# Kernel optimization log

Hardware: AMD Instinct MI355X
Metric: run time of the kernel (lower is better)

Reference implementation:

```python
import jax, jax.numpy as jnp
import numpy as np

N_NODES = 10000
N_EDGES = 320000
MUL = 32            # multiplicity of each input/output irrep
RADIAL = 8          # edge scalar (radial basis) dim
HID = 64            # fc_neurons widths
NUM_NEIGHBORS = 32.0
MIX = np.pi / 8.0
INV_SQRT2 = 1.0 / np.sqrt(2.0)   # per-path alpha: 2 paths feed each mid irrep
INV_SQRT3 = 1.0 / np.sqrt(3.0)   # w3j(1,1,0) normalization


def setup_inputs() -> dict:
    key = jax.random.key(0)
    ks = jax.random.split(key, 16)
    inp = {
        "node_input": jax.random.normal(ks[0], (N_NODES, 4 * MUL), jnp.float32),  # 32x0e+32x1o flat
        "edge_attr": jax.random.normal(ks[1], (N_EDGES, 4), jnp.float32),          # 1x0e+1x1o (sh l=0,1)
        "edge_scalar_attr": jax.random.uniform(ks[2], (N_EDGES, RADIAL), jnp.float32),
        # first linear: 32x0e+32x1o -> (32x0e+32x1o) + (32x0e+32x1o); columns [:MUL]=conv path, [MUL:]=self path
        "W1_0e": jax.random.normal(ks[3], (MUL, 2 * MUL), jnp.float32),
        "W1_1o": jax.random.normal(ks[4], (MUL, 2 * MUL), jnp.float32),
        # radial MLP
        "W_mlp1": jax.random.normal(ks[5], (RADIAL, HID), jnp.float32),
        "W_mlp2": jax.random.normal(ks[6], (HID, HID), jnp.float32),
        # per-instruction 'uvu' path weights (mul_v = 1 squeezed): shape (HID, MUL)
        "Wp_00": jax.random.normal(ks[7], (HID, MUL), jnp.float32),  # 0e x 0e -> 0e
        "Wp_01": jax.random.normal(ks[8], (HID, MUL), jnp.float32),  # 0e x 1o -> 1o
        "Wp_10": jax.random.normal(ks[9], (HID, MUL), jnp.float32),  # 1o x 0e -> 1o
        "Wp_11": jax.random.normal(ks[10], (HID, MUL), jnp.float32), # 1o x 1o -> 0e
        # final linear: 64x0e+64x1o -> 32x0e+32x1o
        "W2_0e": jax.random.normal(ks[11], (2 * MUL, MUL), jnp.float32),
        "W2_1o": jax.random.normal(ks[12], (2 * MUL, MUL), jnp.float32),
        "edge_src": jax.random.randint(ks[13], (N_EDGES,), 0, N_NODES, jnp.int32),
        "edge_dst": jax.random.randint(ks[14], (N_EDGES,), 0, N_NODES, jnp.int32),
    }
    return inp


def _forward(node_input, edge_attr, edge_scalar_attr,
             W1_0e, W1_1o, W_mlp1, W_mlp2,
             Wp_00, Wp_01, Wp_10, Wp_11, W2_0e, W2_1o,
             edge_src, edge_dst):
    N = node_input.shape[0]
    # split flat node features into irrep blocks: 32x0e (N,32), 32x1o (N,32,3)
    x0 = node_input[:, :MUL]
    x1 = node_input[:, MUL:].reshape(N, MUL, 3)

    # ---- equivariant Linear: input -> input + output (fan-in normalized) ----
    f0 = (x0 @ W1_0e) / np.sqrt(MUL)                           # (N, 2*MUL)
    f1 = jnp.einsum('nui,uw->nwi', x1, W1_1o) / np.sqrt(MUL)   # (N, 2*MUL, 3)
    feat0, self0 = f0[:, :MUL], f0[:, MUL:]
    feat1, self1 = f1[:, :MUL], f1[:, MUL:]

    # ---- gather to edges ----
    e0 = feat0[edge_src]        # (E, MUL)
    e1 = feat1[edge_src]        # (E, MUL, 3)
    ea0 = edge_attr[:, :1]      # (E, 1) 0e
    ea1 = edge_attr[:, 1:4]     # (E, 3) 1o

    # ---- radial MLP -> per-edge per-path weights ----
    h = jax.nn.gelu((edge_scalar_attr @ W_mlp1) / np.sqrt(RADIAL))
    h = jax.nn.gelu((h @ W_mlp2) / np.sqrt(HID))               # (E, HID)
    w00 = h @ Wp_00   # (E, MUL)
    w01 = h @ Wp_01
    w10 = h @ Wp_10
    w11 = h @ Wp_11

    # ---- CG tensor product, 'uvu' mode (mul_v = 1) ----
    out0_a = w00 * e0 * ea0                                   # 0e x 0e -> 0e   (E, MUL)
    out0_b = w11 * jnp.sum(e1 * ea1[:, None, :], -1) * INV_SQRT3  # 1o.1o -> 0e
    out1_a = (w01 * e0)[:, :, None] * ea1[:, None, :]         # 0e x 1o -> 1o   (E, MUL, 3)
    out1_b = (w10[:, :, None] * e1) * ea0[:, :, None]         # 1o x 0e -> 1o
    mid0 = jnp.concatenate([out0_a, out0_b], axis=1) * INV_SQRT2  # (E, 2*MUL)   64x0e
    mid1 = jnp.concatenate([out1_a, out1_b], axis=1) * INV_SQRT2  # (E, 2*MUL, 3) 64x1o

    # ---- scatter-add to destination nodes ----
    n0 = jax.ops.segment_sum(mid0, edge_dst, num_segments=N) / np.sqrt(NUM_NEIGHBORS)
    n1 = jax.ops.segment_sum(mid1, edge_dst, num_segments=N) / np.sqrt(NUM_NEIGHBORS)

    # ---- final equivariant Linear: 64x0e+64x1o -> 32x0e+32x1o ----
    conv0 = (n0 @ W2_0e) / np.sqrt(2 * MUL)                    # (N, MUL)
    conv1 = jnp.einsum('nui,uw->nwi', n1, W2_1o) / np.sqrt(2 * MUL)  # (N, MUL, 3)

    c, s = np.cos(MIX), np.sin(MIX)
    y0 = c * self0 + s * conv0
    y1 = c * self1 + s * conv1
    return jnp.concatenate([y0, y1.reshape(N, MUL * 3)], axis=1)  # (N, 128)


def reference(node_input, edge_attr, edge_scalar_attr,
              W1_0e, W1_1o, W_mlp1, W_mlp2,
              Wp_00, Wp_01, Wp_10, Wp_11, W2_0e, W2_1o,
              edge_src, edge_dst):
    return _forward(node_input, edge_attr, edge_scalar_attr,
                    W1_0e, W1_1o, W_mlp1, W_mlp2,
                    Wp_00, Wp_01, Wp_10, Wp_11, W2_0e, W2_1o,
                    edge_src, edge_dst)
```

## Files before the change

### kernel.cpp

```cpp
#include <hip/hip_runtime.h>

typedef unsigned int uint32;
typedef __attribute__((ext_vector_type(4))) float f32x4;
typedef __attribute__((ext_vector_type(8))) _Float16 halfx8;
typedef __attribute__((ext_vector_type(4))) uint32 uint32x4;

#define N_NODES 10000
#define N_EDGES 320000

#define SC_W1      0.17677669529663687f
#define SC_MLP1    0.35355339059327373f
#define SC_MLP2    0.125f
#define INV_SQRT3  0.5773502691896258f
#define COS_MIX    0.9238795325112867f
#define SIN_CONV   0.04783542904563623f

#define WS_FEATP 0
#define I_CNT    1280000
#define I_OFF    1290016
#define U_REC    1300032
#define U_WF     2580032
#define U_WBUF   2587200

__device__ __forceinline__ uint32 f2bf(float x) {
    uint32 u = __float_as_uint(x);
    return (u + 0x7fffu + ((u >> 16) & 1u)) >> 16;
}
__device__ __forceinline__ uint32 pack_bf2(float a, float b) {
    return f2bf(a) | (f2bf(b) << 16);
}
__device__ __forceinline__ uint32 packh2(float a, float b) {
    _Float16 ha = (_Float16)a, hb = (_Float16)b;
    return (uint32)__builtin_bit_cast(unsigned short, ha) |
           ((uint32)__builtin_bit_cast(unsigned short, hb) << 16);
}
__device__ __forceinline__ unsigned short h16(float x) {
    _Float16 h = (_Float16)x;
    return __builtin_bit_cast(unsigned short, h);
}
__device__ __forceinline__ float gelu_fast(float x) {
    float x2 = x * x;
    float z = x * __builtin_fmaf(0.03567740814f, x2, 0.7978845608f);
    float E = __builtin_amdgcn_exp2f(z * -2.885390082f);
    return x * __builtin_amdgcn_rcpf(1.0f + E);
}

#define K1_NODE_BLOCKS 2500
#define K1_CNT_BLOCKS  1250
#define K1_PREP_BLOCKS 7
__global__ __launch_bounds__(256) void k1_fused(
        const float* __restrict__ x,
        const float* __restrict__ W1_0e, const float* __restrict__ W1_1o,
        const int* __restrict__ edge_dst, int* __restrict__ cnt,
        const float* __restrict__ Wm1, const float* __restrict__ Wm2,
        const float* __restrict__ Wp00, const float* __restrict__ Wp01,
        const float* __restrict__ Wp10, const float* __restrict__ Wp11,
        uint32* __restrict__ wf,
        float* __restrict__ featp, float* __restrict__ out) {
    int b = blockIdx.x;
    if (b < K1_NODE_BLOCKS) {
        __shared__ float xrow[4][128];
        int wv = threadIdx.x >> 6, lane = threadIdx.x & 63;
        int node = b * 4 + wv;
        float2 v = *(const float2*)(x + (size_t)node * 128 + lane * 2);
        xrow[wv][lane * 2]     = v.x;
        xrow[wv][lane * 2 + 1] = v.y;
        __syncthreads();
        const float* sx = xrow[wv];
        int w = lane;
        float f0 = 0.f, f1x = 0.f, f1y = 0.f, f1z = 0.f;
#pragma unroll
        for (int u = 0; u < 32; ++u) {
            float w0 = W1_0e[u * 64 + w];
            float w1 = W1_1o[u * 64 + w];
            f0  += sx[u] * w0;
            f1x += sx[32 + u * 3 + 0] * w1;
            f1y += sx[32 + u * 3 + 1] * w1;
            f1z += sx[32 + u * 3 + 2] * w1;
        }
        f0 *= SC_W1; f1x *= SC_W1; f1y *= SC_W1; f1z *= SC_W1;
        if (w < 32) {
            featp[node * 128 + w]      = f0;
            featp[node * 128 + 32 + w] = f1x;
            featp[node * 128 + 64 + w] = f1y;
            featp[node * 128 + 96 + w] = f1z;
        } else {
            int ww = w - 32;
            out[node * 128 + ww] = COS_MIX * f0;
            out[node * 128 + 32 + ww * 3 + 0] = COS_MIX * f1x;
            out[node * 128 + 32 + ww * 3 + 1] = COS_MIX * f1y;
            out[node * 128 + 32 + ww * 3 + 2] = COS_MIX * f1z;
        }
    } else if (b < K1_NODE_BLOCKS + K1_CNT_BLOCKS) {
        int e = (b - K1_NODE_BLOCKS) * 256 + threadIdx.x;
        atomicAdd(&cnt[edge_dst[e]], 1);
    } else {
        int gid = (b - K1_NODE_BLOCKS - K1_CNT_BLOCKS) * 256 + threadIdx.x;
        int f = gid >> 6, lane = gid & 63;
        int kq = (lane >> 4) * 8;
        int c15 = lane & 15;
        float vals[8];
        if (f < 4) {
            int c = 16 * f + c15;
#pragma unroll
            for (int j = 0; j < 8; ++j) { int k = kq + j; vals[j] = (k < 8) ? Wm1[k * 64 + c] : 0.f; }
        } else if (f < 12) {
            int idx = f - 4, nt = idx >> 1, ks = idx & 1;
            int c = 16 * nt + c15;
#pragma unroll
            for (int j = 0; j < 8; ++j) { int k = 32 * ks + kq + j; vals[j] = Wm2[k * 64 + c]; }
        } else {
            int idx = f - 12, nt = idx >> 1, ks = idx & 1;
            int c = 16 * nt + c15;
            int u = c & 31, m = c >> 5;
            const float* W = (m == 0) ? Wp00 : (m == 1) ? Wp01 : (m == 2) ? Wp10 : Wp11;
            float sc = (m == 3) ? 0.125f * INV_SQRT3 : 0.125f;
#pragma unroll
            for (int j = 0; j < 8; ++j) { int k = 32 * ks + kq + j; vals[j] = W[k * 32 + u] * sc; }
        }
        uint32* o = wf + f * 256 + lane * 4;
#pragma unroll
        for (int w = 0; w < 4; ++w) o[w] = packh2(vals[2 * w], vals[2 * w + 1]);
    }
}

__global__ __launch_bounds__(1024) void csr_scan(const int* __restrict__ cnt,
                                                 int* __restrict__ off) {
    __shared__ int partial[1024];
    int t = threadIdx.x;
    const int CHUNK = 10;
    int base = t * CHUNK;
    int s = 0;
#pragma unroll
    for (int j = 0; j < CHUNK; ++j) {
        int idx = base + j;
        s += (idx < N_NODES) ? cnt[idx] : 0;
    }
    partial[t] = s;
    __syncthreads();
    for (int o = 1; o < 1024; o <<= 1) {
        int v = partial[t];
        int add = (t >= o) ? partial[t - o] : 0;
        __syncthreads();
        partial[t] = v + add;
        __syncthreads();
    }
    int run = (t > 0) ? partial[t - 1] : 0;
    for (int j = 0; j < CHUNK; ++j) {
        int idx = base + j;
        if (idx < N_NODES) {
            off[idx] = run;
            run += cnt[idx];
        }
    }
    if (t == 1023) off[N_NODES] = run;
}

#define MLP_BLOCKS 1250
__global__ __launch_bounds__(256) void mlp_scatter(
        const float* __restrict__ edge_scalar, const float* __restrict__ edge_attr,
        const int* __restrict__ src_in, const int* __restrict__ dst_in,
        int* __restrict__ off,
        const uint32* __restrict__ wf,
        uint32* __restrict__ wbuf, uint4* __restrict__ rec) {
    __shared__ unsigned short sh[4][1024];
    __shared__ float eaxs[4][16];
    __shared__ int   poss[4][16];
    int lane = threadIdx.x & 63;
    int wvq = threadIdx.x >> 6;
    int wave_id = blockIdx.x * 4 + wvq;
    int kq = (lane >> 4) * 8;
    int r15 = lane & 15;

    const uint32x4* wfp = (const uint32x4*)wf;
    halfx8 wb1[4], wb2[4][2], wbp[8][2];
#pragma unroll
    for (int nt = 0; nt < 4; ++nt)
        wb1[nt] = __builtin_bit_cast(halfx8, wfp[nt * 64 + lane]);
#pragma unroll
    for (int nt = 0; nt < 4; ++nt)
#pragma unroll
        for (int ks = 0; ks < 2; ++ks)
            wb2[nt][ks] = __builtin_bit_cast(halfx8, wfp[(4 + nt * 2 + ks) * 64 + lane]);
#pragma unroll
    for (int nt = 0; nt < 8; ++nt)
#pragma unroll
        for (int ks = 0; ks < 2; ++ks)
            wbp[nt][ks] = __builtin_bit_cast(halfx8, wfp[(12 + nt * 2 + ks) * 64 + lane]);

    const f32x4 z4 = {0.f, 0.f, 0.f, 0.f};
    unsigned short* shw = sh[wvq];

    for (int g = wave_id; g < N_EDGES / 16; g += MLP_BLOCKS * 4) {
        int e0 = g * 16;

        halfx8 a0 = (halfx8)0;
        if (lane < 16) {
            int e = e0 + lane;
            const float* esp = edge_scalar + (size_t)e * 8;
            float4 p = *(const float4*)esp;
            float4 q = *(const float4*)(esp + 4);
            float4 av = *(const float4*)(edge_attr + (size_t)e * 4);
            int dn = dst_in[e];
            int sn = src_in[e];
            int pos = atomicAdd(&off[dn], 1);
            poss[wvq][lane] = pos;
            eaxs[wvq][lane] = av.x;
            uint4 rv;
            rv.x = __float_as_uint(av.y);
            rv.y = __float_as_uint(av.z);
            rv.z = __float_as_uint(av.w);
            rv.w = (uint32)sn;
            rec[pos] = rv;
            a0[0] = (_Float16)p.x; a0[1] = (_Float16)p.y;
            a0[2] = (_Float16)p.z; a0[3] = (_Float16)p.w;
            a0[4] = (_Float16)q.x; a0[5] = (_Float16)q.y;
            a0[6] = (_Float16)q.z; a0[7] = (_Float16)q.w;
        }

        f32x4 acc1[4];
#pragma unroll
        for (int nt = 0; nt < 4; ++nt)
            acc1[nt] = __builtin_amdgcn_mfma_f32_16x16x32_f16(a0, wb1[nt], z4, 0, 0, 0);
#pragma unroll
        for (int nt = 0; nt < 4; ++nt)
#pragma unroll
            for (int i = 0; i < 4; ++i) {
                float gv = gelu_fast(acc1[nt][i] * SC_MLP1);
                int rr = (lane >> 4) * 4 + i;
                int ix = rr * 64 + 16 * nt + r15;
                shw[ix ^ ((rr & 7) << 3)] = h16(gv);
            }
        halfx8 a1[2];
#pragma unroll
        for (int ks = 0; ks < 2; ++ks) {
            int ix = r15 * 64 + 32 * ks + kq;
            a1[ks] = __builtin_bit_cast(halfx8,
                       *(const uint32x4*)&shw[ix ^ ((r15 & 7) << 3)]);
        }

        f32x4 acc2[4];
#pragma unroll
        for (int nt = 0; nt < 4; ++nt) {
            acc2[nt] = __builtin_amdgcn_mfma_f32_16x16x32_f16(a1[0], wb2[nt][0], z4, 0, 0, 0);
            acc2[nt] = __builtin_amdgcn_mfma_f32_16x16x32_f16(a1[1], wb2[nt][1], acc2[nt], 0, 0, 0);
        }
#pragma unroll
        for (int nt = 0; nt < 4; ++nt)
#pragma unroll
            for (int i = 0; i < 4; ++i) {
                float gv = gelu_fast(acc2[nt][i] * SC_MLP2);
                int rr = (lane >> 4) * 4 + i;
                int ix = rr * 64 + 16 * nt + r15;
                shw[ix ^ ((rr & 7) << 3)] = h16(gv);
            }
        halfx8 a2[2];
#pragma unroll
        for (int ks = 0; ks < 2; ++ks) {
            int ix = r15 * 64 + 32 * ks + kq;
            a2[ks] = __builtin_bit_cast(halfx8,
                       *(const uint32x4*)&shw[ix ^ ((r15 & 7) << 3)]);
        }

        f32x4 accp[8];
#pragma unroll
        for (int nt = 0; nt < 8; ++nt) {
            accp[nt] = __builtin_amdgcn_mfma_f32_16x16x32_f16(a2[0], wbp[nt][0], z4, 0, 0, 0);
            accp[nt] = __builtin_amdgcn_mfma_f32_16x16x32_f16(a2[1], wbp[nt][1], accp[nt], 0, 0, 0);
        }

#pragma unroll
        for (int i = 0; i < 4; ++i) {
            int rr = (lane >> 4) * 4 + i;
            float eax = eaxs[wvq][rr];
            int pos = poss[wvq][rr];
            uint32* wrow = wbuf + (size_t)pos * 64 + r15;
            wrow[0]  = pack_bf2(accp[0][i] * eax, accp[2][i]);
            wrow[16] = pack_bf2(accp[1][i] * eax, accp[3][i]);
            wrow[32] = pack_bf2(accp[4][i] * eax, accp[6][i]);
            wrow[48] = pack_bf2(accp[5][i] * eax, accp[7][i]);
        }
    }
}

__global__ __launch_bounds__(256) void gather(const int* __restrict__ off,
                                              const int* __restrict__ cnt,
                                              const uint4* __restrict__ rec,
                                              const uint32* __restrict__ wbuf,
                                              const float* __restrict__ featp,
                                              const float* __restrict__ W2_0e,
                                              const float* __restrict__ W2_1o,
                                              float* __restrict__ out) {
    int wv = threadIdx.x >> 6;
    int lane = threadIdx.x & 63;
    int node = blockIdx.x * 4 + wv;
    int u = lane & 31;
    int half = lane >> 5;

    int end = __builtin_amdgcn_readfirstlane(off[node]);
    int beg = end - __builtin_amdgcn_readfirstlane(cnt[node]);

    float a0acc = 0.f, a1x = 0.f, a1y = 0.f, a1z = 0.f;
    int offA = u + half * 32, offB = 64 + u, offC = 96 + u;

    for (int i0 = beg; i0 < end; i0 += 64) {
        int nn = end - i0;
        if (nn > 64) nn = 64;
        int idx = i0 + ((lane < nn) ? lane : 0);
        uint4 rv = rec[idx];
        int eyv = (int)rv.x, ezv = (int)rv.y, ewv = (int)rv.z, svv = (int)rv.w;
        for (int j0 = 0; j0 < nn; j0 += 4) {
            uint32 wl_[4];
            float fa_[4], fb_[4], fc_[4], ey_[4], ez_[4], ew_[4];
#pragma unroll
            for (int t = 0; t < 4; ++t) {
                int j = j0 + t;
                int jc = (j < nn) ? j : nn - 1;
                ey_[t] = __uint_as_float((uint32)__builtin_amdgcn_readlane(eyv, jc));
                ez_[t] = __uint_as_float((uint32)__builtin_amdgcn_readlane(ezv, jc));
                ew_[t] = __uint_as_float((uint32)__builtin_amdgcn_readlane(ewv, jc));
                int s  = __builtin_amdgcn_readlane(svv, jc);
                uint32 wl = wbuf[(size_t)(i0 + jc) * 64 + lane];
                wl_[t] = (j < nn) ? wl : 0u;
                const float* fp = featp + (size_t)s * 128;
                fa_[t] = fp[offA];
                fb_[t] = fp[offB];
                fc_[t] = fp[offC];
            }
#pragma unroll
            for (int t = 0; t < 4; ++t) {
                float wa = __uint_as_float(wl_[t] << 16);
                float wb = __uint_as_float(wl_[t] & 0xffff0000u);
                float va = half ? ey_[t] : 1.0f;
                float vb = half ? ez_[t] : 0.0f;
                float vc = half ? ew_[t] : 0.0f;
                float dot = fa_[t] * va + fb_[t] * vb + fc_[t] * vc;
                float w0s = half ? wb : wa;
                a0acc += w0s * dot;
                float m  = half ? wa : wb * fa_[t];
                float vx = half ? fa_[t] : ey_[t];
                float vy = half ? fb_[t] : ez_[t];
                float vz = half ? fc_[t] : ew_[t];
                a1x += m * vx; a1y += m * vy; a1z += m * vz;
            }
        }
    }

    __shared__ float red[4][256];
    float* r = red[wv];
    int c = (half << 5) + u;
    r[c] = a0acc;
    int b = 64 + c * 3;
    r[b] = a1x; r[b + 1] = a1y; r[b + 2] = a1z;
    __syncthreads();

    if (half == 0) {
        float acc = 0.f;
#pragma unroll 8
        for (int w = 0; w < 64; ++w) acc += r[w] * W2_0e[w * 32 + u];
        int o = node * 128 + u;
        out[o] = out[o] + SIN_CONV * acc;
    } else {
        float c0 = 0.f, c1 = 0.f, c2 = 0.f;
#pragma unroll 8
        for (int w = 0; w < 64; ++w) {
            float bw = W2_1o[w * 32 + u];
            c0 += r[64 + w * 3 + 0] * bw;
            c1 += r[64 + w * 3 + 1] * bw;
            c2 += r[64 + w * 3 + 2] * bw;
        }
        int o = node * 128 + 32 + u * 3;
        out[o + 0] = out[o + 0] + SIN_CONV * c0;
        out[o + 1] = out[o + 1] + SIN_CONV * c1;
        out[o + 2] = out[o + 2] + SIN_CONV * c2;
    }
}

extern "C" void kernel_launch(void* const* d_in, const int* in_sizes, int n_in,
                              void* d_out, int out_size, void* d_ws, size_t ws_size,
                              hipStream_t stream) {
    const float* node_input  = (const float*)d_in[0];
    const float* edge_attr   = (const float*)d_in[1];
    const float* edge_scalar = (const float*)d_in[2];
    const float* W1_0e       = (const float*)d_in[3];
    const float* W1_1o       = (const float*)d_in[4];
    const float* W_mlp1      = (const float*)d_in[5];
    const float* W_mlp2      = (const float*)d_in[6];
    const float* Wp00        = (const float*)d_in[7];
    const float* Wp01        = (const float*)d_in[8];
    const float* Wp10        = (const float*)d_in[9];
    const float* Wp11        = (const float*)d_in[10];
    const float* W2_0e       = (const float*)d_in[11];
    const float* W2_1o       = (const float*)d_in[12];
    const int*   edge_src    = (const int*)d_in[13];
    const int*   edge_dst    = (const int*)d_in[14];
    float* ws   = (float*)d_ws;
    int*   wsI  = (int*)d_ws;
    uint32* wsU = (uint32*)d_ws;
    uint4* recp = (uint4*)(wsU + U_REC);
    float* outp = (float*)d_out;

    hipMemsetAsync(wsI + I_CNT, 0, (N_NODES + 1) * sizeof(int), stream);

    k1_fused<<<K1_NODE_BLOCKS + K1_CNT_BLOCKS + K1_PREP_BLOCKS, 256, 0, stream>>>(
        node_input, W1_0e, W1_1o, edge_dst, wsI + I_CNT,
        W_mlp1, W_mlp2, Wp00, Wp01, Wp10, Wp11, wsU + U_WF, ws + WS_FEATP, outp);
    csr_scan<<<1, 1024, 0, stream>>>(wsI + I_CNT, wsI + I_OFF);
    mlp_scatter<<<MLP_BLOCKS, 256, 0, stream>>>(edge_scalar, edge_attr,
                                                edge_src, edge_dst, wsI + I_OFF,
                                                wsU + U_WF, wsU + U_WBUF, recp);
    gather<<<N_NODES / 4, 256, 0, stream>>>(wsI + I_OFF, wsI + I_CNT, recp,
                                            wsU + U_WBUF, ws + WS_FEATP,
                                            W2_0e, W2_1o, outp);
}
```

Before: 126.3 us.

## Split edge MLP into reorder pass and CSR-ordered MLP pass

The fused MLP+scatter kernel is split in two. A lightweight reorder kernel does the atomic CSR placement and writes fp16 radial inputs and packed edge attributes into sorted slots. The MLP kernel then reads and writes wbuf contiguously in CSR order, so its output stores are coalesced instead of scattered. The edge_attr x scaling moves into the gather kernel. The cost is an extra kernel launch and an extra round trip of radial data through global memory, and y/z are stored as bf16, which lowers their precision.

```diff
diff --git a/kernel.cpp b/kernel.cpp
--- a/kernel.cpp
+++ b/kernel.cpp
@@ -156,16 +156,34 @@
     if (t == 1023) off[N_NODES] = run;
 }
 
-#define MLP_BLOCKS 1250
-__global__ __launch_bounds__(256) void mlp_scatter(
+__global__ __launch_bounds__(256) void reorder(
         const float* __restrict__ edge_scalar, const float* __restrict__ edge_attr,
         const int* __restrict__ src_in, const int* __restrict__ dst_in,
         int* __restrict__ off,
-        const uint32* __restrict__ wf,
         uint32* __restrict__ wbuf, uint4* __restrict__ rec) {
+    int e = blockIdx.x * 256 + threadIdx.x;
+    float4 p = *(const float4*)(edge_scalar + (size_t)e * 8);
+    float4 q = *(const float4*)(edge_scalar + (size_t)e * 8 + 4);
+    float4 av = *(const float4*)(edge_attr + (size_t)e * 4);
+    int sn = src_in[e];
+    int dn = dst_in[e];
+    int pos = atomicAdd(&off[dn], 1);
+    uint4 h;
+    h.x = packh2(p.x, p.y); h.y = packh2(p.z, p.w);
+    h.z = packh2(q.x, q.y); h.w = packh2(q.z, q.w);
+    *(uint4*)(wbuf + (size_t)pos * 64) = h;
+    uint4 rv;
+    rv.x = pack_bf2(av.y, av.z);
+    rv.y = __float_as_uint(av.w);
+    rv.z = __float_as_uint(av.x);
+    rv.w = (uint32)sn;
+    rec[pos] = rv;
+}
+
+#define MLP_BLOCKS 2500
+__global__ __launch_bounds__(256) void mlp_pass(const uint32* __restrict__ wf,
+                                                uint32* __restrict__ wbuf) {
     __shared__ unsigned short sh[4][1024];
-    __shared__ float eaxs[4][16];
-    __shared__ int   poss[4][16];
     int lane = threadIdx.x & 63;
     int wvq = threadIdx.x >> 6;
     int wave_id = blockIdx.x * 4 + wvq;
@@ -192,30 +210,12 @@
     unsigned short* shw = sh[wvq];
 
     for (int g = wave_id; g < N_EDGES / 16; g += MLP_BLOCKS * 4) {
-        int e0 = g * 16;
+        int p0 = g * 16;
 
         halfx8 a0 = (halfx8)0;
         if (lane < 16) {
-            int e = e0 + lane;
-            const float* esp = edge_scalar + (size_t)e * 8;
-            float4 p = *(const float4*)esp;
-            float4 q = *(const float4*)(esp + 4);
-            float4 av = *(const float4*)(edge_attr + (size_t)e * 4);
-            int dn = dst_in[e];
-            int sn = src_in[e];
-            int pos = atomicAdd(&off[dn], 1);
-            poss[wvq][lane] = pos;
-            eaxs[wvq][lane] = av.x;
-            uint4 rv;
-            rv.x = __float_as_uint(av.y);
-            rv.y = __float_as_uint(av.z);
-            rv.z = __float_as_uint(av.w);
-            rv.w = (uint32)sn;
-            rec[pos] = rv;
-            a0[0] = (_Float16)p.x; a0[1] = (_Float16)p.y;
-            a0[2] = (_Float16)p.z; a0[3] = (_Float16)p.w;
-            a0[4] = (_Float16)q.x; a0[5] = (_Float16)q.y;
-            a0[6] = (_Float16)q.z; a0[7] = (_Float16)q.w;
+            uint4 h = *(const uint4*)(wbuf + (size_t)(p0 + lane) * 64);
+            a0 = __builtin_bit_cast(halfx8, h);
         }
 
         f32x4 acc1[4];
@@ -272,13 +272,11 @@
 #pragma unroll
         for (int i = 0; i < 4; ++i) {
             int rr = (lane >> 4) * 4 + i;
-            float eax = eaxs[wvq][rr];
-            int pos = poss[wvq][rr];
-            uint32* wrow = wbuf + (size_t)pos * 64 + r15;
-            wrow[0]  = pack_bf2(accp[0][i] * eax, accp[2][i]);
-            wrow[16] = pack_bf2(accp[1][i] * eax, accp[3][i]);
-            wrow[32] = pack_bf2(accp[4][i] * eax, accp[6][i]);
-            wrow[48] = pack_bf2(accp[5][i] * eax, accp[7][i]);
+            uint32* wrow = wbuf + (size_t)(p0 + rr) * 64 + r15;
+            wrow[0]  = pack_bf2(accp[0][i], accp[2][i]);
+            wrow[16] = pack_bf2(accp[1][i], accp[3][i]);
+            wrow[32] = pack_bf2(accp[4][i], accp[6][i]);
+            wrow[48] = pack_bf2(accp[5][i], accp[7][i]);
         }
     }
 }
@@ -308,17 +306,19 @@
         if (nn > 64) nn = 64;
         int idx = i0 + ((lane < nn) ? lane : 0);
         uint4 rv = rec[idx];
-        int eyv = (int)rv.x, ezv = (int)rv.y, ewv = (int)rv.z, svv = (int)rv.w;
+        int yzv = (int)rv.x, ewv = (int)rv.y, exv = (int)rv.z, svv = (int)rv.w;
         for (int j0 = 0; j0 < nn; j0 += 4) {
             uint32 wl_[4];
-            float fa_[4], fb_[4], fc_[4], ey_[4], ez_[4], ew_[4];
+            float fa_[4], fb_[4], fc_[4], ey_[4], ez_[4], ew_[4], ex_[4];
 #pragma unroll
             for (int t = 0; t < 4; ++t) {
                 int j = j0 + t;
                 int jc = (j < nn) ? j : nn - 1;
-                ey_[t] = __uint_as_float((uint32)__builtin_amdgcn_readlane(eyv, jc));
-                ez_[t] = __uint_as_float((uint32)__builtin_amdgcn_readlane(ezv, jc));
+                uint32 yz = (uint32)__builtin_amdgcn_readlane(yzv, jc);
+                ey_[t] = __uint_as_float(yz << 16);
+                ez_[t] = __uint_as_float(yz & 0xffff0000u);
                 ew_[t] = __uint_as_float((uint32)__builtin_amdgcn_readlane(ewv, jc));
+                ex_[t] = __uint_as_float((uint32)__builtin_amdgcn_readlane(exv, jc));
                 int s  = __builtin_amdgcn_readlane(svv, jc);
                 uint32 wl = wbuf[(size_t)(i0 + jc) * 64 + lane];
                 wl_[t] = (j < nn) ? wl : 0u;
@@ -329,7 +329,7 @@
             }
 #pragma unroll
             for (int t = 0; t < 4; ++t) {
-                float wa = __uint_as_float(wl_[t] << 16);
+                float wa = __uint_as_float(wl_[t] << 16) * ex_[t];
                 float wb = __uint_as_float(wl_[t] & 0xffff0000u);
                 float va = half ? ey_[t] : 1.0f;
                 float vb = half ? ez_[t] : 0.0f;
@@ -406,9 +406,9 @@
         node_input, W1_0e, W1_1o, edge_dst, wsI + I_CNT,
         W_mlp1, W_mlp2, Wp00, Wp01, Wp10, Wp11, wsU + U_WF, ws + WS_FEATP, outp);
     csr_scan<<<1, 1024, 0, stream>>>(wsI + I_CNT, wsI + I_OFF);
-    mlp_scatter<<<MLP_BLOCKS, 256, 0, stream>>>(edge_scalar, edge_attr,
-                                                edge_src, edge_dst, wsI + I_OFF,
-                                                wsU + U_WF, wsU + U_WBUF, recp);
+    reorder<<<1250, 256, 0, stream>>>(edge_scalar, edge_attr, edge_src, edge_dst,
+                                      wsI + I_OFF, wsU + U_WBUF, recp);
+    mlp_pass<<<MLP_BLOCKS, 256, 0, stream>>>(wsU + U_WF, wsU + U_WBUF);
     gather<<<N_NODES / 4, 256, 0, stream>>>(wsI + I_OFF, wsI + I_CNT, recp,
                                             wsU + U_WBUF, ws + WS_FEATP,
                                             W2_0e, W2_1o, outp);
```

After: 147.5 us. +16.8%, slower.

## Store per-edge path weights as FP8 and coalesce writes via LDS staging

Applied to the files above, without the earlier changes.

Per-edge path weights in wbuf are now stored as packed FP8 pairs (2 bytes per slot) instead of packed bf16 pairs (4 bytes), halving the intermediate buffer written by mlp_scatter and read by gather. The writes are first staged in shared memory and then emitted as 16-byte vector stores per destination row, replacing scattered 4-byte stores. The gather kernel reads 16-bit entries and unpacks them with the hardware FP8-to-f32 conversion. This cuts memory traffic on the scattered intermediate, but FP8 has much lower precision and range and may breach accuracy tolerance.

```diff
diff --git a/kernel.cpp b/kernel.cpp
--- a/kernel.cpp
+++ b/kernel.cpp
@@ -1,7 +1,9 @@
 #include <hip/hip_runtime.h>
 
 typedef unsigned int uint32;
+typedef unsigned short ushrt;
 typedef __attribute__((ext_vector_type(4))) float f32x4;
+typedef __attribute__((ext_vector_type(2))) float f32x2;
 typedef __attribute__((ext_vector_type(8))) _Float16 halfx8;
 typedef __attribute__((ext_vector_type(4))) uint32 uint32x4;
 
@@ -22,13 +24,6 @@
 #define U_WF     2580032
 #define U_WBUF   2587200
 
-__device__ __forceinline__ uint32 f2bf(float x) {
-    uint32 u = __float_as_uint(x);
-    return (u + 0x7fffu + ((u >> 16) & 1u)) >> 16;
-}
-__device__ __forceinline__ uint32 pack_bf2(float a, float b) {
-    return f2bf(a) | (f2bf(b) << 16);
-}
 __device__ __forceinline__ uint32 packh2(float a, float b) {
     _Float16 ha = (_Float16)a, hb = (_Float16)b;
     return (uint32)__builtin_bit_cast(unsigned short, ha) |
@@ -37,6 +32,9 @@
 __device__ __forceinline__ unsigned short h16(float x) {
     _Float16 h = (_Float16)x;
     return __builtin_bit_cast(unsigned short, h);
+}
+__device__ __forceinline__ unsigned short pack_fp8_2(float a, float b) {
+    return (unsigned short)(__builtin_amdgcn_cvt_pk_fp8_f32(a, b, 0, false) & 0xffff);
 }
 __device__ __forceinline__ float gelu_fast(float x) {
     float x2 = x * x;
@@ -164,6 +162,7 @@
         const uint32* __restrict__ wf,
         uint32* __restrict__ wbuf, uint4* __restrict__ rec) {
     __shared__ unsigned short sh[4][1024];
+    __shared__ uint32 ob[4][512];
     __shared__ float eaxs[4][16];
     __shared__ int   poss[4][16];
     int lane = threadIdx.x & 63;
@@ -190,6 +189,8 @@
 
     const f32x4 z4 = {0.f, 0.f, 0.f, 0.f};
     unsigned short* shw = sh[wvq];
+    uint32* obw = ob[wvq];
+    unsigned short* obw16 = (unsigned short*)obw;
 
     for (int g = wave_id; g < N_EDGES / 16; g += MLP_BLOCKS * 4) {
         int e0 = g * 16;
@@ -273,12 +274,19 @@
         for (int i = 0; i < 4; ++i) {
             int rr = (lane >> 4) * 4 + i;
             float eax = eaxs[wvq][rr];
-            int pos = poss[wvq][rr];
-            uint32* wrow = wbuf + (size_t)pos * 64 + r15;
-            wrow[0]  = pack_bf2(accp[0][i] * eax, accp[2][i]);
-            wrow[16] = pack_bf2(accp[1][i] * eax, accp[3][i]);
-            wrow[32] = pack_bf2(accp[4][i] * eax, accp[6][i]);
-            wrow[48] = pack_bf2(accp[5][i] * eax, accp[7][i]);
+            unsigned short* orow = obw16 + rr * 64;
+            orow[r15]      = pack_fp8_2(accp[0][i] * eax, accp[2][i]);
+            orow[16 + r15] = pack_fp8_2(accp[1][i] * eax, accp[3][i]);
+            orow[32 + r15] = pack_fp8_2(accp[4][i] * eax, accp[6][i]);
+            orow[48 + r15] = pack_fp8_2(accp[5][i] * eax, accp[7][i]);
+        }
+#pragma unroll
+        for (int pass = 0; pass < 2; ++pass) {
+            int r = pass * 8 + (lane >> 3);
+            int pos = poss[wvq][r];
+            int c4 = (lane & 7) * 4;
+            uint32x4 v = *(const uint32x4*)&obw[r * 32 + c4];
+            *(uint32x4*)(wbuf + (size_t)pos * 32 + c4) = v;
         }
     }
 }
@@ -302,6 +310,8 @@
 
     float a0acc = 0.f, a1x = 0.f, a1y = 0.f, a1z = 0.f;
     int offA = u + half * 32, offB = 64 + u, offC = 96 + u;
+    const ushrt* wbuf16 = (const ushrt*)wbuf;
+    int uslot = (half << 5) + u;
 
     for (int i0 = beg; i0 < end; i0 += 64) {
         int nn = end - i0;
@@ -320,7 +330,7 @@
                 ez_[t] = __uint_as_float((uint32)__builtin_amdgcn_readlane(ezv, jc));
                 ew_[t] = __uint_as_float((uint32)__builtin_amdgcn_readlane(ewv, jc));
                 int s  = __builtin_amdgcn_readlane(svv, jc);
-                uint32 wl = wbuf[(size_t)(i0 + jc) * 64 + lane];
+                uint32 wl = (uint32)wbuf16[(size_t)(i0 + jc) * 64 + uslot];
                 wl_[t] = (j < nn) ? wl : 0u;
                 const float* fp = featp + (size_t)s * 128;
                 fa_[t] = fp[offA];
@@ -329,8 +339,9 @@
             }
 #pragma unroll
             for (int t = 0; t < 4; ++t) {
-                float wa = __uint_as_float(wl_[t] << 16);
-                float wb = __uint_as_float(wl_[t] & 0xffff0000u);
+                f32x2 wab = __builtin_amdgcn_cvt_pk_f32_fp8((int)wl_[t], false);
+                float wa = wab.x;
+                float wb = wab.y;
                 float va = half ? ey_[t] : 1.0f;
                 float vb = half ? ez_[t] : 0.0f;
                 float vc = half ? ew_[t] : 0.0f;
```

After: 121.5 us. -3.8%, faster.
